# Performance work log

Hardware: AMD Instinct MI355X
Metric: run time of the kernel (lower is better)

Reference implementation:

```python
import jax, jax.numpy as jnp
import numpy as np
from jax import lax

DN = ('NCHW', 'OIHW', 'NCHW')


def squash(x):
    # x: [..., d]; squared-norm over last dim
    sq = jnp.sum(x * x, axis=-1, keepdims=True)
    return sq * x / ((1.0 + sq) * jnp.sqrt(sq))


def setup_inputs() -> dict:
    key = jax.random.key(0)
    ks = jax.random.split(key, 6)
    B = 512
    x = jax.random.normal(ks[0], (B, 1, 28, 28), dtype=jnp.float32)
    conv1_w = jax.random.normal(ks[1], (256, 1, 9, 9), dtype=jnp.float32) * 0.05
    conv1_b = jnp.zeros((256,), dtype=jnp.float32)
    conv2_w = jax.random.normal(ks[2], (256, 256, 9, 9), dtype=jnp.float32) * 0.02
    conv2_b = jnp.zeros((256,), dtype=jnp.float32)
    # W: [num_routes=1152, num_capsules=10, out_channels=16, in_channels=8]
    W = jax.random.normal(ks[3], (1152, 10, 16, 8), dtype=jnp.float32)
    return {"x": x, "conv1_w": conv1_w, "conv1_b": conv1_b,
            "conv2_w": conv2_w, "conv2_b": conv2_b, "W": W}


def reference(x, conv1_w, conv1_b, conv2_w, conv2_b, W):
    B = x.shape[0]
    # conv1 + ReLU: [B,1,28,28] -> [B,256,20,20]
    h = lax.conv_general_dilated(x, conv1_w, (1, 1), 'VALID', dimension_numbers=DN)
    h = jax.nn.relu(h + conv1_b[None, :, None, None])
    # primary capsule conv: [B,256,20,20] -> [B,256,6,6], stride 2
    h = lax.conv_general_dilated(h, conv2_w, (2, 2), 'VALID', dimension_numbers=DN)
    h = h + conv2_b[None, :, None, None]
    # reshape to capsules [B, 1152, 8] (matches torch .view on NCHW) and squash
    u = squash(h.reshape(B, -1, 8))
    # u_hat[b,r,c,o] = W[r,c,o,i] @ u[b,r,i]
    u_hat = jnp.einsum('rcoi,bri->brco', W, u)  # [B,1152,10,16]
    R, C = W.shape[0], W.shape[1]
    b_ij = jnp.zeros((R, C), dtype=x.dtype)
    num_iterations = 3
    for it in range(num_iterations):
        c_ij = jax.nn.softmax(b_ij, axis=0)          # softmax over routes
        s_j = jnp.einsum('rc,brco->bco', c_ij, u_hat)  # [B,10,16]
        v_j = squash(s_j)
        if it < num_iterations - 1:
            a_ij = jnp.einsum('brco,bco->brc', u_hat, v_j)  # agreement
            b_ij = b_ij + a_ij.mean(axis=0)
    return v_j  # [B,10,16]
```

## Files before the change

kernel.cpp:

```cpp
#include <hip/hip_runtime.h>
#include <stdint.h>


typedef unsigned short u16;
typedef unsigned int u32;
typedef short short8 __attribute__((ext_vector_type(8)));
typedef float f32x4 __attribute__((ext_vector_type(4)));

__device__ __forceinline__ u16 f2bf(float f) {
  u32 u = __float_as_uint(f);
  return (u16)((u + 0x7FFFu + ((u >> 16) & 1u)) >> 16);
}

__device__ __forceinline__ void gload_lds16(const void* g, void* l) {
  __builtin_amdgcn_global_load_lds(
      (const __attribute__((address_space(1))) void*)g,
      (__attribute__((address_space(3))) void*)l, 16, 0, 0);
}

__global__ __launch_bounds__(256) void conv1_kernel(
    const float* __restrict__ x, const float* __restrict__ w1,
    const float* __restrict__ b1, u16* __restrict__ hT) {
  int b = blockIdx.x;
  int co0 = blockIdx.y * 128;
  int t = threadIdx.x;
  if (t >= 200) return;
  int oh = t / 10, ow0 = (t % 10) * 2;
  const float* xb = x + (size_t)b * 784;
  float patch[9][10];
#pragma unroll
  for (int kh = 0; kh < 9; ++kh)
#pragma unroll
    for (int j = 0; j < 10; ++j) patch[kh][j] = xb[(oh + kh) * 28 + ow0 + j];
  u16* hb = hT + ((size_t)b * 400 + oh * 20 + ow0) * 256 + co0;
  for (int c8 = 0; c8 < 16; ++c8) {
    u16 o0[8], o1[8];
#pragma unroll
    for (int cc = 0; cc < 8; ++cc) {
      int co = co0 + c8 * 8 + cc;
      const float* wc = w1 + co * 81;
      float a0 = 0.f, a1 = 0.f;
#pragma unroll
      for (int kh = 0; kh < 9; ++kh)
#pragma unroll
        for (int kw = 0; kw < 9; ++kw) {
          float wv = wc[kh * 9 + kw];
          a0 = fmaf(wv, patch[kh][kw], a0);
          a1 = fmaf(wv, patch[kh][kw + 1], a1);
        }
      float bias = b1[co];
      o0[cc] = f2bf(fmaxf(a0 + bias, 0.f));
      o1[cc] = f2bf(fmaxf(a1 + bias, 0.f));
    }
    *(uint4*)(hb + c8 * 8) = *(uint4*)o0;
    *(uint4*)(hb + 256 + c8 * 8) = *(uint4*)o1;
  }
}

__global__ __launch_bounds__(256) void prep_w2_kernel(
    const float* __restrict__ w2, u16* __restrict__ A2) {
  __shared__ u16 tl[81 * 264];
  int co = blockIdx.x;
  int tid = threadIdx.x;
  const float* wp = w2 + (size_t)co * 20736;
#pragma unroll
  for (int k = 0; k < 81; ++k) {
    int li = k * 256 + tid;
    int ci = li / 81, t = li - ci * 81;
    tl[t * 264 + ci] = f2bf(wp[li]);
  }
  __syncthreads();
  u16* op = A2 + (size_t)co * 20736;
  for (int oc = tid; oc < 2592; oc += 256) {
    int k0 = oc * 8;
    int t = k0 >> 8, ci0 = k0 & 255;
    *(uint4*)(op + k0) = *(const uint4*)&tl[t * 264 + ci0];
  }
}

__global__ __launch_bounds__(256) void init_u_kernel(
    const float* __restrict__ b2, float* __restrict__ u) {
  int i = blockIdx.x * 256 + threadIdx.x;
  int b = i / 2304, j0 = (i - b * 2304) * 4;
  float4 v;
  v.x = b2[j0 / 36]; v.y = b2[(j0 + 1) / 36];
  v.z = b2[(j0 + 2) / 36]; v.w = b2[(j0 + 3) / 36];
  *(float4*)(u + (size_t)b * 9216 + j0) = v;
}

__global__ __launch_bounds__(512, 2) void conv2_kernel(
    const u16* __restrict__ hT, const u16* __restrict__ A2,
    float* __restrict__ u) {
  __shared__ __align__(16) u16 lds_[65536];
  char* const ldsc = (char*)lds_;
  const int bx = blockIdx.x;
  const int nbk = bx % 72, kz = bx / 72;
  const int n0 = nbk * 256;
  const int tid = threadIdx.x;
  const int lane = tid & 63, w = tid >> 6;
  const int wr = w >> 2, wc = w & 3;
  const int fr = lane & 15, fg = lane >> 4;
  const int w1024 = w * 1024;

  const int rA = tid >> 3;
  const int qsrc = (tid & 7) ^ (rA & 7);
  const int AbaseT = rA * 20736 + qsrc * 8;
  int Bb[4];
#pragma unroll
  for (int rg = 0; rg < 4; ++rg) {
    int n = n0 + rg * 64 + rA;
    int b = n / 36, sp = n - b * 36, oh = sp / 6, ow = sp - oh * 6;
    Bb[rg] = (b * 400 + oh * 40 + ow * 2) * 256 + qsrc * 8;
  }

  const int kx0 = (fg ^ (fr & 7)) << 4;
  const int kx1 = ((4 + fg) ^ (fr & 7)) << 4;
  const int wr16384 = wr * 16384;
  const int bh16384 = 32768 + (wc >> 1) * 16384;
  const int brow0 = (wc & 1) * 64;

  f32x4 acc[8][4] = {};
  short8 areg[4][2], breg[2][2];

#define STAGE_A(E, H, GT) do {                                               \
    char* p_ = ldsc + (E) * 65536 + (H) * 16384 + w1024;                     \
    gload_lds16(A2 + AbaseT + ((H) * 2 + 0) * 1327104 + (GT) * 64, p_);      \
    gload_lds16(A2 + AbaseT + ((H) * 2 + 1) * 1327104 + (GT) * 64, p_ + 8192); \
  } while (0)
#define STAGE_B(E, H, BOFF) do {                                             \
    char* p_ = ldsc + (E) * 65536 + 32768 + (H) * 16384 + w1024;             \
    gload_lds16(hT + Bb[(H) * 2 + 0] + (BOFF), p_);                          \
    gload_lds16(hT + Bb[(H) * 2 + 1] + (BOFF), p_ + 8192);                   \
  } while (0)
#define STAGE_ALL(E, GT) do {                                                \
    int tap_ = (GT) >> 2;                                                    \
    int kh_ = tap_ / 9, kw_ = tap_ - kh_ * 9;                                \
    int bo_ = (kh_ * 20 + kw_) * 256 + ((GT) & 3) * 64;                      \
    STAGE_A(E, 0, GT); STAGE_B(E, 0, bo_);                                   \
    STAGE_B(E, 1, bo_); STAGE_A(E, 1, GT);                                   \
  } while (0)
#define RD_A(D, MH) do { _Pragma("unroll")                                   \
    for (int mr = 0; mr < 4; ++mr) {                                         \
      const char* r_ = ldsc + (D) * 65536 + wr16384 +                        \
                       ((MH) * 64 + mr * 16 + fr) * 128;                     \
      areg[mr][0] = *(const short8*)(r_ + kx0);                              \
      areg[mr][1] = *(const short8*)(r_ + kx1);                              \
    } } while (0)
#define RD_B(D, NH) do { _Pragma("unroll")                                   \
    for (int nr = 0; nr < 2; ++nr) {                                         \
      const char* r_ = ldsc + (D) * 65536 + bh16384 +                        \
                       (brow0 + (NH) * 32 + nr * 16 + fr) * 128;             \
      breg[nr][0] = *(const short8*)(r_ + kx0);                              \
      breg[nr][1] = *(const short8*)(r_ + kx1);                              \
    } } while (0)
#define MM16(MH, NH) do {                                                    \
    __builtin_amdgcn_s_setprio(1);                                           \
    _Pragma("unroll") for (int mr = 0; mr < 4; ++mr)                         \
    _Pragma("unroll") for (int nr = 0; nr < 2; ++nr) {                       \
      acc[(MH)*4+mr][(NH)*2+nr] = __builtin_amdgcn_mfma_f32_16x16x32_bf16(   \
          areg[mr][0], breg[nr][0], acc[(MH)*4+mr][(NH)*2+nr], 0, 0, 0);     \
      acc[(MH)*4+mr][(NH)*2+nr] = __builtin_amdgcn_mfma_f32_16x16x32_bf16(   \
          areg[mr][1], breg[nr][1], acc[(MH)*4+mr][(NH)*2+nr], 0, 0, 0);     \
    }                                                                        \
    __builtin_amdgcn_s_setprio(0);                                           \
  } while (0)
#define BAR_PRE() do {                                                       \
    __builtin_amdgcn_s_barrier();                                            \
    asm volatile("s_waitcnt lgkmcnt(0)" ::: "memory");                       \
    __builtin_amdgcn_sched_barrier(0);                                       \
  } while (0)
#define BAR_ONLY() do {                                                      \
    __builtin_amdgcn_s_barrier();                                            \
    asm volatile("" ::: "memory");                                           \
  } while (0)
#define VM_BAR(N) do {                                                       \
    asm volatile("s_waitcnt vmcnt(" N ")" ::: "memory");                     \
    __builtin_amdgcn_s_barrier();                                            \
    asm volatile("" ::: "memory");                                           \
  } while (0)
#define TILE_STD(T, D, E) do {                                               \
    RD_A(D, 0); RD_B(D, 0);                                                  \
    STAGE_ALL(E, kz * 108 + (T) + 1);                                        \
    BAR_PRE(); MM16(0, 0); BAR_ONLY();                                       \
    RD_B(D, 1);                                                              \
    BAR_PRE(); MM16(0, 1); VM_BAR("8");                                      \
    RD_A(D, 1);                                                              \
    BAR_PRE(); MM16(1, 1); BAR_ONLY();                                       \
    RD_B(D, 0);                                                              \
    BAR_PRE(); MM16(1, 0); VM_BAR("2");                                      \
  } while (0)
#define TILE_LAST(D) do {                                                    \
    RD_A(D, 0); RD_B(D, 0);                                                  \
    BAR_PRE(); MM16(0, 0); BAR_ONLY();                                       \
    RD_B(D, 1);                                                              \
    BAR_PRE(); MM16(0, 1); VM_BAR("0");                                      \
    RD_A(D, 1);                                                              \
    BAR_PRE(); MM16(1, 1); BAR_ONLY();                                       \
    RD_B(D, 0);                                                              \
    BAR_PRE(); MM16(1, 0);                                                   \
  } while (0)

  STAGE_ALL(0, kz * 108);
  asm volatile("s_waitcnt vmcnt(2)" ::: "memory");
  __builtin_amdgcn_s_barrier();
  asm volatile("" ::: "memory");

  for (int tt = 0; tt < 53; ++tt) {
    TILE_STD(2 * tt, 0, 1);
    TILE_STD(2 * tt + 1, 1, 0);
  }
  TILE_STD(106, 0, 1);
  TILE_LAST(1);

#pragma unroll
  for (int nf = 0; nf < 4; ++nf) {
    int cn = n0 + wc * 64 + nf * 16 + fr;
    int ob = cn / 36;
    int os = cn - ob * 36;
    float* op = u + (size_t)ob * 9216 + os;
#pragma unroll
    for (int mf = 0; mf < 8; ++mf) {
      int row0 = wr * 128 + mf * 16 + fg * 4;
#pragma unroll
      for (int qq = 0; qq < 4; ++qq)
        atomicAdd(op + (row0 + qq) * 36, acc[mf][nf][qq]);
    }
  }
#undef STAGE_A
#undef STAGE_B
#undef STAGE_ALL
#undef RD_A
#undef RD_B
#undef MM16
#undef BAR_PRE
#undef BAR_ONLY
#undef VM_BAR
#undef TILE_STD
#undef TILE_LAST
}

__global__ __launch_bounds__(256) void squash_kernel(
    const float* __restrict__ u, u16* __restrict__ ub) {
  int idx = blockIdx.x * 256 + threadIdx.x;
  const float* up = u + (size_t)idx * 8;
  float4 a = *(const float4*)up;
  float4 c = *(const float4*)(up + 4);
  float sq = a.x * a.x + a.y * a.y + a.z * a.z + a.w * a.w +
             c.x * c.x + c.y * c.y + c.z * c.z + c.w * c.w;
  float f = sqrtf(sq) / (1.0f + sq);
  u16 o[8];
  o[0] = f2bf(a.x * f); o[1] = f2bf(a.y * f);
  o[2] = f2bf(a.z * f); o[3] = f2bf(a.w * f);
  o[4] = f2bf(c.x * f); o[5] = f2bf(c.y * f);
  o[6] = f2bf(c.z * f); o[7] = f2bf(c.w * f);
  *(uint4*)(ub + (size_t)idx * 8) = *(uint4*)o;
}

__global__ __launch_bounds__(256) void transp_kernel(
    const u16* __restrict__ ub, u16* __restrict__ ubT) {
  __shared__ u16 tl[64][72];
  int ri0 = blockIdx.x * 64, b0 = blockIdx.y * 64;
  int tid = threadIdx.x;
  int br = tid >> 2, cq = tid & 3;
  const u16* ip = ub + (size_t)(b0 + br) * 9216 + ri0 + cq * 16;
  uint4 v0 = *(const uint4*)ip;
  uint4 v1 = *(const uint4*)(ip + 8);
  *(uint4*)&tl[br][cq * 16] = v0;
  *(uint4*)&tl[br][cq * 16 + 8] = v1;
  __syncthreads();
  int rr = tid >> 2, cb = tid & 3;
  u16 o0[8], o1[8];
#pragma unroll
  for (int j = 0; j < 8; ++j) {
    o0[j] = tl[cb * 16 + j][rr];
    o1[j] = tl[cb * 16 + 8 + j][rr];
  }
  u16* opp = ubT + (size_t)(ri0 + rr) * 512 + b0 + cb * 16;
  *(uint4*)opp = *(uint4*)o0;
  *(uint4*)(opp + 8) = *(uint4*)o1;
}

__global__ __launch_bounds__(256) void gemm_s_kernel(
    const float* __restrict__ W, const float* __restrict__ bij,
    const u16* __restrict__ ub, float* __restrict__ s) {
  __shared__ __align__(16) u16 Asl[160 * 72];
  __shared__ __align__(16) u16 Bsl[64 * 72];
  __shared__ float smx[10], sinv[10];
  int nb = blockIdx.x & 7, kzi = blockIdx.x >> 3;
  int n0 = nb * 64, k0 = kzi * 256;
  int tid = threadIdx.x;
  int lane = tid & 63, wave = tid >> 6;
  int fr = lane & 15, fg = lane >> 4;

  for (int c = wave; c < 10; c += 4) {
    float mx = -1e30f;
    for (int r = lane; r < 1152; r += 64) mx = fmaxf(mx, bij[r * 10 + c]);
#pragma unroll
    for (int d = 1; d < 64; d <<= 1) mx = fmaxf(mx, __shfl_xor(mx, d, 64));
    float sm = 0.f;
    for (int r = lane; r < 1152; r += 64) sm += expf(bij[r * 10 + c] - mx);
#pragma unroll
    for (int d = 1; d < 64; d <<= 1) sm += __shfl_xor(sm, d, 64);
    if (lane == 0) { smx[c] = mx; sinv[c] = 1.0f / sm; }
  }

  f32x4 acc[10] = {};
#pragma unroll
  for (int st = 0; st < 4; ++st) {
    int kb = k0 + st * 64;
    __syncthreads();
#pragma unroll
    for (int j = 0; j < 5; ++j) {
      int c5 = tid + j * 256;
      int row = c5 >> 3, qq = c5 & 7;
      int cls = row >> 4, o = row & 15;
      int r = (kb + qq * 8) >> 3;
      const float* wp = W + (size_t)r * 1280 + cls * 128 + o * 8;
      float4 w0 = *(const float4*)wp;
      float4 w1 = *(const float4*)(wp + 4);
      float cs = expf(bij[r * 10 + cls] - smx[cls]) * sinv[cls];
      u16 ov[8];
      ov[0] = f2bf(w0.x * cs); ov[1] = f2bf(w0.y * cs);
      ov[2] = f2bf(w0.z * cs); ov[3] = f2bf(w0.w * cs);
      ov[4] = f2bf(w1.x * cs); ov[5] = f2bf(w1.y * cs);
      ov[6] = f2bf(w1.z * cs); ov[7] = f2bf(w1.w * cs);
      *(uint4*)((char*)Asl + row * 144 + qq * 16) = *(uint4*)ov;
    }
#pragma unroll
    for (int j = 0; j < 2; ++j) {
      int c2 = tid + j * 256;
      int row = c2 >> 3, qq = c2 & 7;
      *(uint4*)((char*)Bsl + row * 144 + qq * 16) =
          *(const uint4*)(ub + (size_t)(n0 + row) * 9216 + kb + qq * 8);
    }
    __syncthreads();
#pragma unroll
    for (int s2 = 0; s2 < 2; ++s2) {
      int xg = (s2 * 4 + fg) * 16;
      short8 bf0 = *(const short8*)((char*)Bsl + (wave * 16 + fr) * 144 + xg);
#pragma unroll
      for (int m = 0; m < 10; ++m) {
        short8 af = *(const short8*)((char*)Asl + (m * 16 + fr) * 144 + xg);
        acc[m] = __builtin_amdgcn_mfma_f32_16x16x32_bf16(af, bf0, acc[m], 0, 0, 0);
      }
    }
  }
  int bcol = n0 + wave * 16 + fr;
#pragma unroll
  for (int m = 0; m < 10; ++m)
#pragma unroll
    for (int qq = 0; qq < 4; ++qq)
      atomicAdd(s + (m * 16 + fg * 4 + qq) * 512 + bcol, acc[m][qq]);
}

__global__ __launch_bounds__(256) void squash_v_kernel(
    float* __restrict__ s, u16* __restrict__ vb,
    float* __restrict__ outp, int write_out) {
  int idx = blockIdx.x * 256 + threadIdx.x;
  int c = idx >> 9, b = idx & 511;
  float vals[16];
  float sq = 0.f;
#pragma unroll
  for (int o = 0; o < 16; ++o) {
    float v = s[(c * 16 + o) * 512 + b];
    vals[o] = v;
    sq += v * v;
  }
#pragma unroll
  for (int o = 0; o < 16; ++o) s[(c * 16 + o) * 512 + b] = 0.f;
  float f = sqrtf(sq) / (1.0f + sq);
  if (write_out) {
#pragma unroll
    for (int o = 0; o < 16; ++o) outp[((size_t)b * 10 + c) * 16 + o] = vals[o] * f;
  } else {
#pragma unroll
    for (int o = 0; o < 16; ++o) vb[(c * 16 + o) * 512 + b] = f2bf(vals[o] * f);
  }
}

__global__ __launch_bounds__(256) void gemm_gc_kernel(
    const u16* __restrict__ vb, const u16* __restrict__ ubT,
    const float* __restrict__ W, float* __restrict__ bij) {
  __shared__ __align__(16) u16 Agl[160 * 72];
  __shared__ __align__(16) u16 Bgl[128 * 72];
  __shared__ float Gl[160 * 129];
  int nb = blockIdx.x % 72, kzi = blockIdx.x / 72;
  int n0 = nb * 128, k0 = kzi * 128;
  int tid = threadIdx.x;
  int lane = tid & 63, wave = tid >> 6;
  int fr = lane & 15, fg = lane >> 4;
  f32x4 acc[10][2] = {};
#pragma unroll
  for (int st = 0; st < 2; ++st) {
    int kb = k0 + st * 64;
    __syncthreads();
#pragma unroll
    for (int j = 0; j < 5; ++j) {
      int c5 = tid + j * 256;
      int row = c5 >> 3, qq = c5 & 7;
      *(uint4*)((char*)Agl + row * 144 + qq * 16) =
          *(const uint4*)(vb + (size_t)row * 512 + kb + qq * 8);
    }
#pragma unroll
    for (int j = 0; j < 4; ++j) {
      int c4 = tid + j * 256;
      int row = c4 >> 3, qq = c4 & 7;
      *(uint4*)((char*)Bgl + row * 144 + qq * 16) =
          *(const uint4*)(ubT + (size_t)(n0 + row) * 512 + kb + qq * 8);
    }
    __syncthreads();
#pragma unroll
    for (int s2 = 0; s2 < 2; ++s2) {
      int xg = (s2 * 4 + fg) * 16;
      short8 bfv[2];
#pragma unroll
      for (int nn = 0; nn < 2; ++nn)
        bfv[nn] = *(const short8*)((char*)Bgl + (wave * 32 + nn * 16 + fr) * 144 + xg);
#pragma unroll
      for (int m = 0; m < 10; ++m) {
        short8 af = *(const short8*)((char*)Agl + (m * 16 + fr) * 144 + xg);
#pragma unroll
        for (int nn = 0; nn < 2; ++nn)
          acc[m][nn] = __builtin_amdgcn_mfma_f32_16x16x32_bf16(af, bfv[nn],
                                                              acc[m][nn], 0, 0, 0);
      }
    }
  }
#pragma unroll
  for (int m = 0; m < 10; ++m)
#pragma unroll
    for (int nn = 0; nn < 2; ++nn) {
      int col = wave * 32 + nn * 16 + fr;
#pragma unroll
      for (int qq = 0; qq < 4; ++qq)
        Gl[(m * 16 + fg * 4 + qq) * 129 + col] = acc[m][nn][qq];
    }
  __syncthreads();
  if (tid < 160) {
    int rl = tid / 10, c = tid - rl * 10;
    int r = (n0 >> 3) + rl;
    const float* wp = W + (size_t)r * 1280 + c * 128;
    float a = 0.f;
#pragma unroll 4
    for (int o = 0; o < 16; ++o) {
      const float* gp = &Gl[(c * 16 + o) * 129 + rl * 8];
#pragma unroll
      for (int i = 0; i < 8; ++i) a = fmaf(wp[o * 8 + i], gp[i], a);
    }
    atomicAdd(&bij[r * 10 + c], a * (1.0f / 512.0f));
  }
}

extern "C" void kernel_launch(void* const* d_in, const int* in_sizes, int n_in,
                              void* d_out, int out_size, void* d_ws, size_t ws_size,
                              hipStream_t stream) {
  const float* x  = (const float*)d_in[0];
  const float* w1 = (const float*)d_in[1];
  const float* b1 = (const float*)d_in[2];
  const float* w2 = (const float*)d_in[3];
  const float* b2 = (const float*)d_in[4];
  const float* W  = (const float*)d_in[5];
  char* ws = (char*)d_ws;
  u16*   hT  = (u16*)ws;
  u16*   A2  = (u16*)(ws + 104857600);
  float* u   = (float*)(ws + 115474432);
  float* bij = (float*)(ws + 134348800);
  float* s   = (float*)(ws + 134440960);
  u16*   ub  = (u16*)ws;
  u16*   ubT = (u16*)(ws + 9437184);
  u16*   vb  = (u16*)(ws + 21823488);
  float* out = (float*)d_out;

  hipMemsetAsync(bij, 0, 46080, stream);
  hipMemsetAsync(s, 0, 327680, stream);
  init_u_kernel<<<4608, 256, 0, stream>>>(b2, u);
  conv1_kernel<<<dim3(512, 2), 256, 0, stream>>>(x, w1, b1, hT);
  prep_w2_kernel<<<256, 256, 0, stream>>>(w2, A2);
  conv2_kernel<<<216, 512, 0, stream>>>(hT, A2, u);
  squash_kernel<<<2304, 256, 0, stream>>>(u, ub);
  transp_kernel<<<dim3(144, 8), 256, 0, stream>>>(ub, ubT);
  for (int it = 0; it < 3; ++it) {
    gemm_s_kernel<<<288, 256, 0, stream>>>(W, bij, ub, s);
    squash_v_kernel<<<20, 256, 0, stream>>>(s, vb, out, it == 2 ? 1 : 0);
    if (it < 2) gemm_gc_kernel<<<288, 256, 0, stream>>>(vb, ubT, W, bij);
  }
}
```

Baseline: 619.2 us.

## Switch to fp16 MFMA, 2x2 conv1 register tiling, and separate softmax kernel

```diff
diff --git a/kernel.cpp b/kernel.cpp
--- a/kernel.cpp
+++ b/kernel.cpp
@@ -4,12 +4,13 @@
 
 typedef unsigned short u16;
 typedef unsigned int u32;
-typedef short short8 __attribute__((ext_vector_type(8)));
+typedef _Float16 half8 __attribute__((ext_vector_type(8)));
 typedef float f32x4 __attribute__((ext_vector_type(4)));
 
-__device__ __forceinline__ u16 f2bf(float f) {
-  u32 u = __float_as_uint(f);
-  return (u16)((u + 0x7FFFu + ((u >> 16) & 1u)) >> 16);
+__device__ __forceinline__ u16 f2h(float f) {
+  union { _Float16 h; u16 u; } cv;
+  cv.h = (_Float16)f;
+  return cv.u;
 }
 
 __device__ __forceinline__ void gload_lds16(const void* g, void* l) {
@@ -18,42 +19,56 @@
       (__attribute__((address_space(3))) void*)l, 16, 0, 0);
 }
 
-__global__ __launch_bounds__(256) void conv1_kernel(
+__global__ __launch_bounds__(256, 2) void conv1_kernel(
     const float* __restrict__ x, const float* __restrict__ w1,
     const float* __restrict__ b1, u16* __restrict__ hT) {
-  int b = blockIdx.x;
-  int co0 = blockIdx.y * 128;
   int t = threadIdx.x;
   if (t >= 200) return;
-  int oh = t / 10, ow0 = (t % 10) * 2;
-  const float* xb = x + (size_t)b * 784;
-  float patch[9][10];
-#pragma unroll
-  for (int kh = 0; kh < 9; ++kh)
-#pragma unroll
-    for (int j = 0; j < 10; ++j) patch[kh][j] = xb[(oh + kh) * 28 + ow0 + j];
-  u16* hb = hT + ((size_t)b * 400 + oh * 20 + ow0) * 256 + co0;
+  int bloc = t / 100, pos = t - bloc * 100;
+  int b = blockIdx.x * 2 + bloc;
+  int co0 = blockIdx.y * 128;
+  int oh2 = pos / 10, ow2 = pos - oh2 * 10;
+  const float* xb = x + (size_t)b * 784 + (2 * oh2) * 28 + 2 * ow2;
+  float patch[10][10];
+#pragma unroll
+  for (int ky = 0; ky < 10; ++ky)
+#pragma unroll
+    for (int kx = 0; kx < 10; ++kx) patch[ky][kx] = xb[ky * 28 + kx];
+  u16* hb = hT + ((size_t)b * 400 + (2 * oh2) * 20 + 2 * ow2) * 256 + co0;
   for (int c8 = 0; c8 < 16; ++c8) {
-    u16 o0[8], o1[8];
+    u32 q00[4], q01[4], q10[4], q11[4];
 #pragma unroll
     for (int cc = 0; cc < 8; ++cc) {
       int co = co0 + c8 * 8 + cc;
       const float* wc = w1 + co * 81;
-      float a0 = 0.f, a1 = 0.f;
-#pragma unroll
-      for (int kh = 0; kh < 9; ++kh)
-#pragma unroll
-        for (int kw = 0; kw < 9; ++kw) {
-          float wv = wc[kh * 9 + kw];
-          a0 = fmaf(wv, patch[kh][kw], a0);
-          a1 = fmaf(wv, patch[kh][kw + 1], a1);
+      float a00 = 0.f, a01 = 0.f, a10 = 0.f, a11 = 0.f;
+#pragma unroll
+      for (int ky = 0; ky < 9; ++ky)
+#pragma unroll
+        for (int kx = 0; kx < 9; ++kx) {
+          float wv = wc[ky * 9 + kx];
+          a00 = fmaf(wv, patch[ky][kx], a00);
+          a01 = fmaf(wv, patch[ky][kx + 1], a01);
+          a10 = fmaf(wv, patch[ky + 1][kx], a10);
+          a11 = fmaf(wv, patch[ky + 1][kx + 1], a11);
         }
       float bias = b1[co];
-      o0[cc] = f2bf(fmaxf(a0 + bias, 0.f));
-      o1[cc] = f2bf(fmaxf(a1 + bias, 0.f));
-    }
-    *(uint4*)(hb + c8 * 8) = *(uint4*)o0;
-    *(uint4*)(hb + 256 + c8 * 8) = *(uint4*)o1;
+      u32 v00 = f2h(fmaxf(a00 + bias, 0.f));
+      u32 v01 = f2h(fmaxf(a01 + bias, 0.f));
+      u32 v10 = f2h(fmaxf(a10 + bias, 0.f));
+      u32 v11 = f2h(fmaxf(a11 + bias, 0.f));
+      if (cc & 1) {
+        q00[cc >> 1] |= v00 << 16; q01[cc >> 1] |= v01 << 16;
+        q10[cc >> 1] |= v10 << 16; q11[cc >> 1] |= v11 << 16;
+      } else {
+        q00[cc >> 1] = v00; q01[cc >> 1] = v01;
+        q10[cc >> 1] = v10; q11[cc >> 1] = v11;
+      }
+    }
+    *(uint4*)(hb + c8 * 8)        = make_uint4(q00[0], q00[1], q00[2], q00[3]);
+    *(uint4*)(hb + 256 + c8 * 8)  = make_uint4(q01[0], q01[1], q01[2], q01[3]);
+    *(uint4*)(hb + 5120 + c8 * 8) = make_uint4(q10[0], q10[1], q10[2], q10[3]);
+    *(uint4*)(hb + 5376 + c8 * 8) = make_uint4(q11[0], q11[1], q11[2], q11[3]);
   }
 }
 
@@ -67,7 +82,7 @@
   for (int k = 0; k < 81; ++k) {
     int li = k * 256 + tid;
     int ci = li / 81, t = li - ci * 81;
-    tl[t * 264 + ci] = f2bf(wp[li]);
+    tl[t * 264 + ci] = f2h(wp[li]);
   }
   __syncthreads();
   u16* op = A2 + (size_t)co * 20736;
@@ -120,7 +135,7 @@
   const int brow0 = (wc & 1) * 64;
 
   f32x4 acc[8][4] = {};
-  short8 areg[4][2], breg[2][2];
+  half8 areg[4][2], breg[2][2];
 
 #define STAGE_A(E, H, GT) do {                                               \
     char* p_ = ldsc + (E) * 65536 + (H) * 16384 + w1024;                     \
@@ -143,23 +158,23 @@
     for (int mr = 0; mr < 4; ++mr) {                                         \
       const char* r_ = ldsc + (D) * 65536 + wr16384 +                        \
                        ((MH) * 64 + mr * 16 + fr) * 128;                     \
-      areg[mr][0] = *(const short8*)(r_ + kx0);                              \
-      areg[mr][1] = *(const short8*)(r_ + kx1);                              \
+      areg[mr][0] = *(const half8*)(r_ + kx0);                               \
+      areg[mr][1] = *(const half8*)(r_ + kx1);                               \
     } } while (0)
 #define RD_B(D, NH) do { _Pragma("unroll")                                   \
     for (int nr = 0; nr < 2; ++nr) {                                         \
       const char* r_ = ldsc + (D) * 65536 + bh16384 +                        \
                        (brow0 + (NH) * 32 + nr * 16 + fr) * 128;             \
-      breg[nr][0] = *(const short8*)(r_ + kx0);                              \
-      breg[nr][1] = *(const short8*)(r_ + kx1);                              \
+      breg[nr][0] = *(const half8*)(r_ + kx0);                               \
+      breg[nr][1] = *(const half8*)(r_ + kx1);                               \
     } } while (0)
 #define MM16(MH, NH) do {                                                    \
     __builtin_amdgcn_s_setprio(1);                                           \
     _Pragma("unroll") for (int mr = 0; mr < 4; ++mr)                         \
     _Pragma("unroll") for (int nr = 0; nr < 2; ++nr) {                       \
-      acc[(MH)*4+mr][(NH)*2+nr] = __builtin_amdgcn_mfma_f32_16x16x32_bf16(   \
+      acc[(MH)*4+mr][(NH)*2+nr] = __builtin_amdgcn_mfma_f32_16x16x32_f16(    \
           areg[mr][0], breg[nr][0], acc[(MH)*4+mr][(NH)*2+nr], 0, 0, 0);     \
-      acc[(MH)*4+mr][(NH)*2+nr] = __builtin_amdgcn_mfma_f32_16x16x32_bf16(   \
+      acc[(MH)*4+mr][(NH)*2+nr] = __builtin_amdgcn_mfma_f32_16x16x32_f16(    \
           areg[mr][1], breg[nr][1], acc[(MH)*4+mr][(NH)*2+nr], 0, 0, 0);     \
     }                                                                        \
     __builtin_amdgcn_s_setprio(0);                                           \
@@ -249,10 +264,10 @@
              c.x * c.x + c.y * c.y + c.z * c.z + c.w * c.w;
   float f = sqrtf(sq) / (1.0f + sq);
   u16 o[8];
-  o[0] = f2bf(a.x * f); o[1] = f2bf(a.y * f);
-  o[2] = f2bf(a.z * f); o[3] = f2bf(a.w * f);
-  o[4] = f2bf(c.x * f); o[5] = f2bf(c.y * f);
-  o[6] = f2bf(c.z * f); o[7] = f2bf(c.w * f);
+  o[0] = f2h(a.x * f); o[1] = f2h(a.y * f);
+  o[2] = f2h(a.z * f); o[3] = f2h(a.w * f);
+  o[4] = f2h(c.x * f); o[5] = f2h(c.y * f);
+  o[6] = f2h(c.z * f); o[7] = f2h(c.w * f);
   *(uint4*)(ub + (size_t)idx * 8) = *(uint4*)o;
 }
 
@@ -280,29 +295,44 @@
   *(uint4*)(opp + 8) = *(uint4*)o1;
 }
 
+__global__ __launch_bounds__(256) void softmax_c_kernel(
+    const float* __restrict__ bij, float* __restrict__ cT) {
+  int c = blockIdx.x;
+  int tid = threadIdx.x;
+  __shared__ float red[256];
+  float mx = -1e30f;
+  for (int r = tid; r < 1152; r += 256) mx = fmaxf(mx, bij[r * 10 + c]);
+  red[tid] = mx;
+  __syncthreads();
+  for (int s = 128; s > 0; s >>= 1) {
+    if (tid < s) red[tid] = fmaxf(red[tid], red[tid + s]);
+    __syncthreads();
+  }
+  mx = red[0];
+  __syncthreads();
+  float sum = 0.f;
+  for (int r = tid; r < 1152; r += 256) sum += expf(bij[r * 10 + c] - mx);
+  red[tid] = sum;
+  __syncthreads();
+  for (int s = 128; s > 0; s >>= 1) {
+    if (tid < s) red[tid] += red[tid + s];
+    __syncthreads();
+  }
+  float inv = 1.0f / red[0];
+  for (int r = tid; r < 1152; r += 256)
+    cT[c * 1152 + r] = expf(bij[r * 10 + c] - mx) * inv;
+}
+
 __global__ __launch_bounds__(256) void gemm_s_kernel(
-    const float* __restrict__ W, const float* __restrict__ bij,
+    const float* __restrict__ W, const float* __restrict__ cT,
     const u16* __restrict__ ub, float* __restrict__ s) {
   __shared__ __align__(16) u16 Asl[160 * 72];
   __shared__ __align__(16) u16 Bsl[64 * 72];
-  __shared__ float smx[10], sinv[10];
   int nb = blockIdx.x & 7, kzi = blockIdx.x >> 3;
   int n0 = nb * 64, k0 = kzi * 256;
   int tid = threadIdx.x;
   int lane = tid & 63, wave = tid >> 6;
   int fr = lane & 15, fg = lane >> 4;
-
-  for (int c = wave; c < 10; c += 4) {
-    float mx = -1e30f;
-    for (int r = lane; r < 1152; r += 64) mx = fmaxf(mx, bij[r * 10 + c]);
-#pragma unroll
-    for (int d = 1; d < 64; d <<= 1) mx = fmaxf(mx, __shfl_xor(mx, d, 64));
-    float sm = 0.f;
-    for (int r = lane; r < 1152; r += 64) sm += expf(bij[r * 10 + c] - mx);
-#pragma unroll
-    for (int d = 1; d < 64; d <<= 1) sm += __shfl_xor(sm, d, 64);
-    if (lane == 0) { smx[c] = mx; sinv[c] = 1.0f / sm; }
-  }
 
   f32x4 acc[10] = {};
 #pragma unroll
@@ -318,12 +348,12 @@
       const float* wp = W + (size_t)r * 1280 + cls * 128 + o * 8;
       float4 w0 = *(const float4*)wp;
       float4 w1 = *(const float4*)(wp + 4);
-      float cs = expf(bij[r * 10 + cls] - smx[cls]) * sinv[cls];
+      float cs = cT[cls * 1152 + r] * 512.0f;
       u16 ov[8];
-      ov[0] = f2bf(w0.x * cs); ov[1] = f2bf(w0.y * cs);
-      ov[2] = f2bf(w0.z * cs); ov[3] = f2bf(w0.w * cs);
-      ov[4] = f2bf(w1.x * cs); ov[5] = f2bf(w1.y * cs);
-      ov[6] = f2bf(w1.z * cs); ov[7] = f2bf(w1.w * cs);
+      ov[0] = f2h(w0.x * cs); ov[1] = f2h(w0.y * cs);
+      ov[2] = f2h(w0.z * cs); ov[3] = f2h(w0.w * cs);
+      ov[4] = f2h(w1.x * cs); ov[5] = f2h(w1.y * cs);
+      ov[6] = f2h(w1.z * cs); ov[7] = f2h(w1.w * cs);
       *(uint4*)((char*)Asl + row * 144 + qq * 16) = *(uint4*)ov;
     }
 #pragma unroll
@@ -337,11 +367,11 @@
 #pragma unroll
     for (int s2 = 0; s2 < 2; ++s2) {
       int xg = (s2 * 4 + fg) * 16;
-      short8 bf0 = *(const short8*)((char*)Bsl + (wave * 16 + fr) * 144 + xg);
+      half8 bf0 = *(const half8*)((char*)Bsl + (wave * 16 + fr) * 144 + xg);
 #pragma unroll
       for (int m = 0; m < 10; ++m) {
-        short8 af = *(const short8*)((char*)Asl + (m * 16 + fr) * 144 + xg);
-        acc[m] = __builtin_amdgcn_mfma_f32_16x16x32_bf16(af, bf0, acc[m], 0, 0, 0);
+        half8 af = *(const half8*)((char*)Asl + (m * 16 + fr) * 144 + xg);
+        acc[m] = __builtin_amdgcn_mfma_f32_16x16x32_f16(af, bf0, acc[m], 0, 0, 0);
       }
     }
   }
@@ -362,7 +392,7 @@
   float sq = 0.f;
 #pragma unroll
   for (int o = 0; o < 16; ++o) {
-    float v = s[(c * 16 + o) * 512 + b];
+    float v = s[(c * 16 + o) * 512 + b] * (1.0f / 512.0f);
     vals[o] = v;
     sq += v * v;
   }
@@ -374,7 +404,8 @@
     for (int o = 0; o < 16; ++o) outp[((size_t)b * 10 + c) * 16 + o] = vals[o] * f;
   } else {
 #pragma unroll
-    for (int o = 0; o < 16; ++o) vb[(c * 16 + o) * 512 + b] = f2bf(vals[o] * f);
+    for (int o = 0; o < 16; ++o)
+      vb[(c * 16 + o) * 512 + b] = f2h(vals[o] * f * 4096.0f);
   }
 }
 
@@ -412,17 +443,17 @@
 #pragma unroll
     for (int s2 = 0; s2 < 2; ++s2) {
       int xg = (s2 * 4 + fg) * 16;
-      short8 bfv[2];
+      half8 bfv[2];
 #pragma unroll
       for (int nn = 0; nn < 2; ++nn)
-        bfv[nn] = *(const short8*)((char*)Bgl + (wave * 32 + nn * 16 + fr) * 144 + xg);
+        bfv[nn] = *(const half8*)((char*)Bgl + (wave * 32 + nn * 16 + fr) * 144 + xg);
 #pragma unroll
       for (int m = 0; m < 10; ++m) {
-        short8 af = *(const short8*)((char*)Agl + (m * 16 + fr) * 144 + xg);
+        half8 af = *(const half8*)((char*)Agl + (m * 16 + fr) * 144 + xg);
 #pragma unroll
         for (int nn = 0; nn < 2; ++nn)
-          acc[m][nn] = __builtin_amdgcn_mfma_f32_16x16x32_bf16(af, bfv[nn],
-                                                              acc[m][nn], 0, 0, 0);
+          acc[m][nn] = __builtin_amdgcn_mfma_f32_16x16x32_f16(af, bfv[nn],
+                                                             acc[m][nn], 0, 0, 0);
       }
     }
   }
@@ -447,7 +478,7 @@
 #pragma unroll
       for (int i = 0; i < 8; ++i) a = fmaf(wp[o * 8 + i], gp[i], a);
     }
-    atomicAdd(&bij[r * 10 + c], a * (1.0f / 512.0f));
+    atomicAdd(&bij[r * 10 + c], a * (1.0f / (512.0f * 4096.0f)));
   }
 }
 
@@ -465,6 +496,7 @@
   u16*   A2  = (u16*)(ws + 104857600);
   float* u   = (float*)(ws + 115474432);
   float* bij = (float*)(ws + 134348800);
+  float* cT  = (float*)(ws + 134394880);
   float* s   = (float*)(ws + 134440960);
   u16*   ub  = (u16*)ws;
   u16*   ubT = (u16*)(ws + 9437184);
@@ -474,13 +506,14 @@
   hipMemsetAsync(bij, 0, 46080, stream);
   hipMemsetAsync(s, 0, 327680, stream);
   init_u_kernel<<<4608, 256, 0, stream>>>(b2, u);
-  conv1_kernel<<<dim3(512, 2), 256, 0, stream>>>(x, w1, b1, hT);
+  conv1_kernel<<<dim3(256, 2), 256, 0, stream>>>(x, w1, b1, hT);
   prep_w2_kernel<<<256, 256, 0, stream>>>(w2, A2);
   conv2_kernel<<<216, 512, 0, stream>>>(hT, A2, u);
   squash_kernel<<<2304, 256, 0, stream>>>(u, ub);
   transp_kernel<<<dim3(144, 8), 256, 0, stream>>>(ub, ubT);
   for (int it = 0; it < 3; ++it) {
-    gemm_s_kernel<<<288, 256, 0, stream>>>(W, bij, ub, s);
+    softmax_c_kernel<<<10, 256, 0, stream>>>(bij, cT);
+    gemm_s_kernel<<<288, 256, 0, stream>>>(W, cT, ub, s);
     squash_v_kernel<<<20, 256, 0, stream>>>(s, vb, out, it == 2 ? 1 : 0);
     if (it < 2) gemm_gc_kernel<<<288, 256, 0, stream>>>(vb, ubT, W, bij);
   }
```

After: 642.0 us. +3.7%, slower.
